# Kernel tuning notes

Measured on AMD Instinct MI355X. Metric: run time of the kernel, lower is better.

## Reference

```python
import jax, jax.numpy as jnp
import numpy as np

NUM_GENES = 4000
NUM_PATCHES = 64
EMBED_DIM = 192
NUM_CELLS = 4096


def setup_inputs() -> dict:
    key = jax.random.key(0)
    k1, k2, k3, k4 = jax.random.split(key, 4)
    x = jax.random.normal(k1, (NUM_CELLS, NUM_GENES), dtype=jnp.float32)
    # binary gene->pathway membership mask [num_genes, num_patches]
    mask = jax.random.randint(k2, (NUM_GENES, NUM_PATCHES), 0, 2).astype(jnp.float32)
    W = jax.random.normal(k3, (NUM_GENES, NUM_PATCHES * EMBED_DIM), dtype=jnp.float32) * 0.02
    b = jax.random.normal(k4, (NUM_PATCHES * EMBED_DIM,), dtype=jnp.float32) * 0.02
    return {"x": x, "mask": mask, "W": W, "b": b}


def reference(x, mask, W, b):
    # Expand mask as in __init__: np.repeat(mask, embed_dim, axis=1)
    # -> column j belongs to pathway j // embed_dim.
    mask_rep = jnp.repeat(mask, EMBED_DIM, axis=1)  # [genes, patches*embed]
    # CustomizedLinear: dense matmul with statically masked weight.
    out = x @ (W * mask_rep) + b  # [cells, patches*embed]
    # rearrange 'h (w c) -> h c w' with c = num_patches
    out = out.reshape(NUM_CELLS, EMBED_DIM, NUM_PATCHES).transpose(0, 2, 1)
    # norm_layer=None -> Identity
    return out  # [cells, num_patches, embed_dim]
```

## Files before the change

kernel.cpp:

```cpp
#include <hip/hip_runtime.h>
#include <hip/hip_bf16.h>

#define M_CELLS 4096
#define N_GENES 4000
#define KP      4032
#define NKT     63
#define N_OUT   12288
#define EMB     192
#define NPATCH  64

#define BM 256
#define BN 256
#define BK 64
#define BTILE (BN * BK)

typedef __attribute__((ext_vector_type(8))) short bf16x8_t;
typedef __attribute__((ext_vector_type(8))) unsigned short u16x8_t;
typedef __attribute__((ext_vector_type(16))) float f32x16_t;

__device__ __forceinline__ unsigned short f2bf(float f) {
  __hip_bfloat16 h = __float2bfloat16(f);
  return *reinterpret_cast<unsigned short*>(&h);
}

__device__ __forceinline__ void gll16(const unsigned short* g, unsigned short* l) {
  __builtin_amdgcn_global_load_lds(
      (const __attribute__((address_space(1))) void*)g,
      (__attribute__((address_space(3))) void*)l, 16, 0, 0);
}

__global__ __launch_bounds__(256) void prep_fused(const float* __restrict__ x,
                                                  const float* __restrict__ mask,
                                                  const float* __restrict__ W,
                                                  unsigned short* __restrict__ A,
                                                  unsigned short* __restrict__ Bt) {
  __shared__ unsigned short sT[256 * 72];
  __shared__ float smask[256];
  const int t = threadIdx.x;
  if (blockIdx.x < 1024) {
    const int NG = M_CELLS * (KP / 8);
    for (int g = blockIdx.x * 256 + t; g < NG; g += 1024 * 256) {
      int row = g / (KP / 8);
      int kc  = g - row * (KP / 8);
      int k   = kc * 8;
      u16x8_t v;
      if (k < N_GENES) {
        float4 f0 = *reinterpret_cast<const float4*>(x + (size_t)row * N_GENES + k);
        float4 f1 = *reinterpret_cast<const float4*>(x + (size_t)row * N_GENES + k + 4);
        v[0] = f2bf(f0.x); v[1] = f2bf(f0.y); v[2] = f2bf(f0.z); v[3] = f2bf(f0.w);
        v[4] = f2bf(f1.x); v[5] = f2bf(f1.y); v[6] = f2bf(f1.z); v[7] = f2bf(f1.w);
      } else {
        v = (u16x8_t)0;
      }
      *reinterpret_cast<u16x8_t*>(A + (size_t)row * KP + k) = v;
    }
  } else {
    const int idx = blockIdx.x - 1024;
    const int jb  = idx % 48;
    const int kt  = idx / 48;
    const int q   = t & 63;
    const int o   = t >> 6;
    const int pwbase = (jb * 256) / EMB;
    {
      const int kg_l = t & 63;
      const int pwi  = t >> 6;
      const int kg   = kt * 64 + kg_l;
      const int pw   = pwbase + pwi;
      float mv = 0.f;
      if (kg < N_GENES && pw < NPATCH) mv = mask[kg * NPATCH + pw];
      smask[kg_l * 4 + pwi] = mv;
    }
    __syncthreads();
    const int jbase = jb * 256 + q * 4;
    int pwi_[4];
#pragma unroll
    for (int dj = 0; dj < 4; ++dj) pwi_[dj] = (jbase + dj) / EMB - pwbase;

    u16x8_t hreg[4][2];
#pragma unroll
    for (int hb = 0; hb < 2; ++hb) {
#pragma unroll
      for (int kk8 = 0; kk8 < 8; ++kk8) {
        const int kk = hb * 8 + kk8;
        const int kg = kt * 64 + o * 16 + kk;
        float4 f;
        if (kg < N_GENES) f = *reinterpret_cast<const float4*>(W + (size_t)kg * N_OUT + jbase);
        else              f = make_float4(0.f, 0.f, 0.f, 0.f);
        const float fv[4] = {f.x, f.y, f.z, f.w};
#pragma unroll
        for (int dj = 0; dj < 4; ++dj) {
          float m = smask[(o * 16 + kk) * 4 + pwi_[dj]];
          hreg[dj][hb][kk8] = f2bf(fv[dj] * m);
        }
      }
    }
#pragma unroll
    for (int dj = 0; dj < 4; ++dj) {
      const int jl = q * 4 + dj;
#pragma unroll
      for (int hb = 0; hb < 2; ++hb) {
        const int s = (o * 2 + hb) ^ ((jl >> 2) & 7) ^ ((jl >> 5) & 7);
        *reinterpret_cast<u16x8_t*>(&sT[jl * 72 + s * 8]) = hreg[dj][hb];
      }
    }
    __syncthreads();
#pragma unroll
    for (int it = 0; it < 8; ++it) {
      const int f  = it * 256 + t;
      const int p  = f >> 5, u = f & 31;
      const int el = u >> 3;
      const int r  = el * 64 + p;
      const int s  = (u & 7) ^ ((r >> 2) & 7) ^ ((r >> 5) & 7);
      u16x8_t v = *reinterpret_cast<const u16x8_t*>(&sT[r * 72 + s * 8]);
      const int jp0 = p * EMB + jb * 4;
      const int nt  = jp0 >> 8, c = jp0 & 255;
      *reinterpret_cast<u16x8_t*>(&Bt[(size_t)(nt * NKT + kt) * BTILE + (size_t)c * 64 + u * 8]) = v;
    }
  }
}

#define ABASE(buf, ks) (((buf) * 2 + (ks)) * 8192)
#define BBASE(buf, ks) (32768 + ((buf) * 2 + (ks)) * 8192)

__global__ __launch_bounds__(512, 2) void gemm_bf16(const unsigned short* __restrict__ A,
                                                    const unsigned short* __restrict__ Bt,
                                                    const float* __restrict__ bias,
                                                    float* __restrict__ out) {
  __shared__ unsigned short lds[65536];

  const int tid  = threadIdx.x;
  const int lane = tid & 63;
  const int wid  = tid >> 6;
  const int wm   = wid >> 2;
  const int wn   = wid & 3;
  const int la31 = lane & 31;
  const int hi2  = lane >> 5;

  const int bid = blockIdx.x;
  const int xcd = bid & 7;
  const int l   = bid >> 3;
  const int mt  = l & 15;
  const int nt  = xcd * 6 + (l >> 4);
  const int m0  = mt * BM;
  const int n0  = nt * BN;

  const int abase = (wm * 128 + la31) * 16 + hi2 * 8;
  const int bbase = (wn * 64 + la31) * 16 + hi2 * 8;

  const int srow = tid >> 1;
  const int sk   = (tid & 1) * 8;
  const unsigned short* aS0 = A + (size_t)(m0 + srow) * KP + sk;
  const unsigned short* bS0 = Bt + (size_t)nt * NKT * BTILE + (size_t)srow * 64 + sk;

#define STAGE_A(kt, kh, buf) { \
    gll16(aS0 + (kt) * 64 + (kh) * 32,      &lds[ABASE(buf, kh) + tid * 8]); \
    gll16(aS0 + (kt) * 64 + (kh) * 32 + 16, &lds[ABASE(buf, kh) + 4096 + tid * 8]); }
#define STAGE_B(kt, kh, buf) { \
    gll16(bS0 + (size_t)(kt) * BTILE + (kh) * 32,      &lds[BBASE(buf, kh) + tid * 8]); \
    gll16(bS0 + (size_t)(kt) * BTILE + (kh) * 32 + 16, &lds[BBASE(buf, kh) + 4096 + tid * 8]); }

#define RD_K(buf, ks, K16, AF, BF) { \
    BF[0] = *reinterpret_cast<const bf16x8_t*>(&lds[BBASE(buf, ks) + (K16) * 4096 + bbase]); \
    BF[1] = *reinterpret_cast<const bf16x8_t*>(&lds[BBASE(buf, ks) + (K16) * 4096 + bbase + 512]); \
    _Pragma("unroll") for (int m_ = 0; m_ < 4; ++m_) \
      AF[m_] = *reinterpret_cast<const bf16x8_t*>(&lds[ABASE(buf, ks) + (K16) * 4096 + abase + m_ * 512]); }

#define MM8(AF, BF) \
    __builtin_amdgcn_s_setprio(1); \
    _Pragma("unroll") for (int m_ = 0; m_ < 4; ++m_) \
    _Pragma("unroll") for (int n_ = 0; n_ < 2; ++n_) \
      acc[m_][n_] = __builtin_amdgcn_mfma_f32_32x32x16_bf16(AF[m_], BF[n_], acc[m_][n_], 0, 0, 0); \
    __builtin_amdgcn_s_setprio(0);

#define VMBAR(N) \
    asm volatile("s_waitcnt vmcnt(" #N ")" ::: "memory"); \
    __builtin_amdgcn_s_barrier(); \
    asm volatile("" ::: "memory")

  f32x16_t acc[4][2] = {};
  bf16x8_t af0[4], af1[4], bf0[2], bf1[2];

  STAGE_A(0, 0, 0); STAGE_B(0, 0, 0);
  STAGE_A(0, 1, 0); STAGE_B(0, 1, 0);
  STAGE_A(1, 0, 1); STAGE_B(1, 0, 1);
  VMBAR(8);

  for (int i = 0; i < 31; ++i) {
    const int tb = 2 * i + 1, tc = 2 * i + 2;
    const int td = (tb + 2 <= 62) ? tb + 2 : 62;

    STAGE_A(tb, 1, 1); STAGE_B(tb, 1, 1);
    RD_K(0, 0, 0, af0, bf0); MM8(af0, bf0);
    RD_K(0, 0, 1, af1, bf1); MM8(af1, bf1);
    VMBAR(8);
    STAGE_A(tc, 0, 0); STAGE_B(tc, 0, 0);
    RD_K(0, 1, 0, af0, bf0); MM8(af0, bf0);
    RD_K(0, 1, 1, af1, bf1); MM8(af1, bf1);
    VMBAR(8);
    STAGE_A(tc, 1, 0); STAGE_B(tc, 1, 0);
    RD_K(1, 0, 0, af0, bf0); MM8(af0, bf0);
    RD_K(1, 0, 1, af1, bf1); MM8(af1, bf1);
    VMBAR(8);
    STAGE_A(td, 0, 1); STAGE_B(td, 0, 1);
    RD_K(1, 1, 0, af0, bf0); MM8(af0, bf0);
    RD_K(1, 1, 1, af1, bf1); MM8(af1, bf1);
    VMBAR(8);
  }

  RD_K(0, 0, 0, af0, bf0); MM8(af0, bf0);
  RD_K(0, 0, 1, af1, bf1); MM8(af1, bf1);
  VMBAR(4);
  RD_K(0, 1, 0, af0, bf0); MM8(af0, bf0);
  RD_K(0, 1, 1, af1, bf1); MM8(af1, bf1);
  asm volatile("s_waitcnt vmcnt(0)" ::: "memory");
  __builtin_amdgcn_s_barrier();

#pragma unroll
  for (int ni = 0; ni < 2; ++ni) {
    const int jc = n0 + wn * 64 + ni * 32 + la31;
    const float bv = bias[(jc % EMB) * NPATCH + (jc / EMB)];
#pragma unroll
    for (int mi = 0; mi < 4; ++mi) {
      const int rowb = m0 + wm * 128 + mi * 32 + hi2 * 4;
      float* o = out + (size_t)rowb * N_OUT + jc;
#pragma unroll
      for (int rg = 0; rg < 16; ++rg) {
        const int roff = (rg & 3) + 8 * (rg >> 2);
        o[(size_t)roff * N_OUT] = acc[mi][ni][rg] + bv;
      }
    }
  }
}

__global__ __launch_bounds__(256) void fallback_gemm(const float* __restrict__ x,
                                                     const float* __restrict__ mask,
                                                     const float* __restrict__ W,
                                                     const float* __restrict__ b,
                                                     float* __restrict__ out) {
  __shared__ float sX[64 * 33];
  __shared__ float sB2[32 * 65];
  const int t  = threadIdx.x;
  const int c0 = blockIdx.x * 64;
  const int j0 = blockIdx.y * 64;
  const int tr = t >> 4, tc = t & 15;
  float acc[4][4] = {};
  for (int k0 = 0; k0 < N_GENES; k0 += 32) {
    __syncthreads();
#pragma unroll
    for (int i = 0; i < 8; ++i) {
      int f = i * 256 + t;
      int row = f >> 5, kk = f & 31;
      sX[row * 33 + kk] = x[(size_t)(c0 + row) * N_GENES + k0 + kk];
    }
#pragma unroll
    for (int i = 0; i < 8; ++i) {
      int f = i * 256 + t;
      int kk = f >> 6, cl = f & 63;
      int jp = j0 + cl;
      int jorig = (jp % EMB) * NPATCH + jp / EMB;
      sB2[kk * 65 + cl] = W[(size_t)(k0 + kk) * N_OUT + jorig] * mask[(k0 + kk) * NPATCH + jorig / EMB];
    }
    __syncthreads();
#pragma unroll
    for (int kk = 0; kk < 32; ++kk) {
      float a[4], bb[4];
#pragma unroll
      for (int r = 0; r < 4; ++r) a[r] = sX[(tr * 4 + r) * 33 + kk];
#pragma unroll
      for (int c = 0; c < 4; ++c) bb[c] = sB2[kk * 65 + tc * 4 + c];
#pragma unroll
      for (int r = 0; r < 4; ++r)
#pragma unroll
        for (int c = 0; c < 4; ++c) acc[r][c] += a[r] * bb[c];
    }
  }
#pragma unroll
  for (int r = 0; r < 4; ++r)
#pragma unroll
    for (int c = 0; c < 4; ++c) {
      int jp = j0 + tc * 4 + c;
      int jorig = (jp % EMB) * NPATCH + jp / EMB;
      out[(size_t)(c0 + tr * 4 + r) * N_OUT + jp] = acc[r][c] + b[jorig];
    }
}

extern "C" void kernel_launch(void* const* d_in, const int* in_sizes, int n_in,
                              void* d_out, int out_size, void* d_ws, size_t ws_size,
                              hipStream_t stream) {
  const float* x    = (const float*)d_in[0];
  const float* mask = (const float*)d_in[1];
  const float* W    = (const float*)d_in[2];
  const float* b    = (const float*)d_in[3];
  float* out = (float*)d_out;

  const size_t needA = (size_t)M_CELLS * KP * sizeof(unsigned short);
  const size_t needB = (size_t)N_OUT * KP * sizeof(unsigned short);

  if (ws_size >= needA + needB) {
    unsigned short* Abf = (unsigned short*)d_ws;
    unsigned short* Bt  = (unsigned short*)((char*)d_ws + needA);
    prep_fused<<<4048, 256, 0, stream>>>(x, mask, W, Abf, Bt);
    gemm_bf16<<<768, 512, 0, stream>>>(Abf, Bt, b, out);
  } else {
    fallback_gemm<<<dim3(64, 192), 256, 0, stream>>>(x, mask, W, b, out);
  }
}
```

Before: 495.9 us.

## Software-pipeline LDS fragment reads one step ahead of MFMA issue

Restructures the main loop so each LDS fragment read for the next k-step is issued before the MFMAs of the current step, using two alternating register sets. The loop also waits for fewer outstanding global loads at each barrier, and one read is hoisted into the prologue. The aim is to hide LDS read latency behind matrix-core work. In exchange, register pressure rises, and the tighter vmcnt waits may stall on global loads or race if the counts are wrong.

Measured after the change: 490.6 us. About the same (-1.1%).

```diff
diff --git a/kernel.cpp b/kernel.cpp
--- a/kernel.cpp
+++ b/kernel.cpp
@@ -178,40 +178,51 @@
     asm volatile("" ::: "memory")
 
   f32x16_t acc[4][2] = {};
-  bf16x8_t af0[4], af1[4], bf0[2], bf1[2];
+  bf16x8_t afA[4], afB[4], bfA[2], bfB[2];
 
   STAGE_A(0, 0, 0); STAGE_B(0, 0, 0);
   STAGE_A(0, 1, 0); STAGE_B(0, 1, 0);
   STAGE_A(1, 0, 1); STAGE_B(1, 0, 1);
-  VMBAR(8);
+  VMBAR(4);
+  RD_K(0, 0, 0, afA, bfA);
 
   for (int i = 0; i < 31; ++i) {
     const int tb = 2 * i + 1, tc = 2 * i + 2;
     const int td = (tb + 2 <= 62) ? tb + 2 : 62;
 
     STAGE_A(tb, 1, 1); STAGE_B(tb, 1, 1);
-    RD_K(0, 0, 0, af0, bf0); MM8(af0, bf0);
-    RD_K(0, 0, 1, af1, bf1); MM8(af1, bf1);
-    VMBAR(8);
+    RD_K(0, 0, 1, afB, bfB);
+    MM8(afA, bfA);
+    RD_K(0, 1, 0, afA, bfA);
+    MM8(afB, bfB);
+    VMBAR(4);
     STAGE_A(tc, 0, 0); STAGE_B(tc, 0, 0);
-    RD_K(0, 1, 0, af0, bf0); MM8(af0, bf0);
-    RD_K(0, 1, 1, af1, bf1); MM8(af1, bf1);
-    VMBAR(8);
+    RD_K(0, 1, 1, afB, bfB);
+    MM8(afA, bfA);
+    RD_K(1, 0, 0, afA, bfA);
+    MM8(afB, bfB);
+    VMBAR(4);
     STAGE_A(tc, 1, 0); STAGE_B(tc, 1, 0);
-    RD_K(1, 0, 0, af0, bf0); MM8(af0, bf0);
-    RD_K(1, 0, 1, af1, bf1); MM8(af1, bf1);
-    VMBAR(8);
+    RD_K(1, 0, 1, afB, bfB);
+    MM8(afA, bfA);
+    RD_K(1, 1, 0, afA, bfA);
+    MM8(afB, bfB);
+    VMBAR(4);
     STAGE_A(td, 0, 1); STAGE_B(td, 0, 1);
-    RD_K(1, 1, 0, af0, bf0); MM8(af0, bf0);
-    RD_K(1, 1, 1, af1, bf1); MM8(af1, bf1);
-    VMBAR(8);
-  }
-
-  RD_K(0, 0, 0, af0, bf0); MM8(af0, bf0);
-  RD_K(0, 0, 1, af1, bf1); MM8(af1, bf1);
-  VMBAR(4);
-  RD_K(0, 1, 0, af0, bf0); MM8(af0, bf0);
-  RD_K(0, 1, 1, af1, bf1); MM8(af1, bf1);
+    RD_K(1, 1, 1, afB, bfB);
+    MM8(afA, bfA);
+    RD_K(0, 0, 0, afA, bfA);
+    MM8(afB, bfB);
+    VMBAR(4);
+  }
+
+  RD_K(0, 0, 1, afB, bfB);
+  MM8(afA, bfA);
+  RD_K(0, 1, 0, afA, bfA);
+  MM8(afB, bfB);
+  RD_K(0, 1, 1, afB, bfB);
+  MM8(afA, bfA);
+  MM8(afB, bfB);
   asm volatile("s_waitcnt vmcnt(0)" ::: "memory");
   __builtin_amdgcn_s_barrier();
 
```
